# Kernel tuning notes

Hardware: AMD Instinct MI355X
Metric: run time of the kernel (lower is better)

## Reference

```python
import jax, jax.numpy as jnp
import numpy as np

B, T, C, H, D = 2, 2048, 1024, 16, 64

def setup_inputs() -> dict:
    key = jax.random.key(0)
    ks = jax.random.split(key, 5)
    s = 1.0 / np.sqrt(C)
    return {
        "hidden_states": jax.random.normal(ks[0], (B, T, C), jnp.float32),
        "Wq": jax.random.normal(ks[1], (H, C, D), jnp.float32) * s,
        "Wk": jax.random.normal(ks[2], (H, C, D), jnp.float32) * s,
        "Wv": jax.random.normal(ks[3], (H, C, D), jnp.float32) * s,
        "Wo": jax.random.normal(ks[4], (C, C), jnp.float32) * s,
    }

def reference(hidden_states, Wq, Wk, Wv, Wo):
    x = hidden_states  # (B, T, C)
    q = jnp.einsum("btc,hcd->bhtd", x, Wq)
    k = jnp.einsum("btc,hcd->bhtd", x, Wk)
    v = jnp.einsum("btc,hcd->bhtd", x, Wv)
    scale = 1.0 / jnp.sqrt(jnp.asarray(D, x.dtype))
    scores = jnp.einsum("bhtd,bhsd->bhts", q, k) * scale  # (B,H,T,T)
    Tlen = x.shape[1]
    causal = jnp.tril(jnp.ones((Tlen, Tlen), bool))
    scores = jnp.where(causal, scores, jnp.asarray(-jnp.inf, x.dtype))
    probs = jax.nn.softmax(scores, axis=-1)
    heads = jnp.einsum("bhts,bhsd->bhtd", probs, v)  # (B,H,T,D)
    concat = heads.transpose(0, 2, 1, 3).reshape(x.shape[0], Tlen, H * D)  # (B,T,C)
    return jnp.einsum("btc,oc->bto", concat, Wo)  # output projection (dropout=0)
```

## Files before the change

### kernel.cpp

```cpp
#include <hip/hip_runtime.h>
#include <math.h>

#define B_ 2
#define T_ 2048
#define C_ 1024
#define H_ 16
#define D_ 64

typedef short short8 __attribute__((ext_vector_type(8)));
typedef float f32x4 __attribute__((ext_vector_type(4)));
typedef float f32x16 __attribute__((ext_vector_type(16)));

#define LOG2E 1.44269504088896f

__device__ __forceinline__ unsigned short f2bf(float f) {
    unsigned int u = __float_as_uint(f);
    u += 0x7FFFu + ((u >> 16) & 1u);
    return (unsigned short)(u >> 16);
}

#define NCAST 2560

__global__ __launch_bounds__(256) void prep_all(
    const float* __restrict__ x,  const float* __restrict__ Wq,
    const float* __restrict__ Wk, const float* __restrict__ Wv,
    const float* __restrict__ Wo,
    unsigned short* __restrict__ xb,   unsigned short* __restrict__ Wall,
    unsigned short* __restrict__ wob,  int nX, int nW)
{
    const int bid = blockIdx.x;
    const int tid = threadIdx.x;
    if (bid < NCAST) {
        int i = (bid * 256 + tid) * 8;
        const float* s;
        unsigned short* d;
        if (i < nX) { s = x + i; d = xb + i; }
        else {
            int j = i - nX;
            if (j >= nW) return;
            s = Wo + j; d = wob + j;
        }
        float4 a = *(const float4*)s;
        float4 b = *(const float4*)(s + 4);
        ushort4 o0, o1;
        o0.x = f2bf(a.x); o0.y = f2bf(a.y); o0.z = f2bf(a.z); o0.w = f2bf(a.w);
        o1.x = f2bf(b.x); o1.y = f2bf(b.y); o1.z = f2bf(b.z); o1.w = f2bf(b.w);
        *(ushort4*)d = o0;
        *(ushort4*)(d + 4) = o1;
        return;
    }
    __shared__ float t[64][65];
    const int tb = bid - NCAST;
    const int c0 = (tb & 15) * 64;
    const int h  = (tb >> 4) & 15;
    const int z  = tb >> 8;
    const float* W = (z == 0) ? Wq : (z == 1) ? Wk : Wv;
    unsigned short* Wt = Wall + (size_t)z * H_ * D_ * C_;
    const int r = tid >> 4, c4 = (tid & 15) * 4;
    #pragma unroll
    for (int p = 0; p < 4; p++) {
        int cl = r + p * 16;
        float4 v = *(const float4*)&W[((size_t)h * C_ + c0 + cl) * D_ + c4];
        t[cl][c4 + 0] = v.x; t[cl][c4 + 1] = v.y;
        t[cl][c4 + 2] = v.z; t[cl][c4 + 3] = v.w;
    }
    __syncthreads();
    #pragma unroll
    for (int p = 0; p < 4; p++) {
        int d = r + p * 16;
        ushort4 o;
        o.x = f2bf(t[c4 + 0][d]); o.y = f2bf(t[c4 + 1][d]);
        o.z = f2bf(t[c4 + 2][d]); o.w = f2bf(t[c4 + 3][d]);
        *(ushort4*)&Wt[((size_t)h * D_ + d) * C_ + c0 + c4] = o;
    }
}

__global__ __launch_bounds__(256) void qkv_big(
    const unsigned short* __restrict__ X,
    const unsigned short* __restrict__ Wall,
    unsigned short* __restrict__ Qo,
    unsigned short* __restrict__ Ko,
    unsigned short* __restrict__ Vt)
{
    __shared__ unsigned short As[128][72];
    __shared__ unsigned short Bs[128][72];

    const int m0 = blockIdx.x * 128;
    const int n0 = blockIdx.y * 128;
    const int z  = n0 >> 10;
    const int tid = threadIdx.x;
    const int w = tid >> 6, lane = tid & 63, quad = lane >> 4, l16 = lane & 15;
    const int wm = w & 1, wn = w >> 1;
    const int lrow = tid >> 3, lcol = (tid & 7) * 8;

    f32x4 acc[4][4] = {};

    short8 ar[4], br[4];
    #pragma unroll
    for (int p = 0; p < 4; p++) {
        int r = lrow + p * 32;
        ar[p] = *(const short8*)&X[(size_t)(m0 + r) * C_ + lcol];
        br[p] = *(const short8*)&Wall[(size_t)(n0 + r) * C_ + lcol];
    }

    for (int k0 = 0; k0 < C_; k0 += 64) {
        __syncthreads();
        #pragma unroll
        for (int p = 0; p < 4; p++) {
            int r = lrow + p * 32;
            *(short8*)&As[r][lcol] = ar[p];
            *(short8*)&Bs[r][lcol] = br[p];
        }
        __syncthreads();
        if (k0 + 64 < C_) {
            #pragma unroll
            for (int p = 0; p < 4; p++) {
                int r = lrow + p * 32;
                ar[p] = *(const short8*)&X[(size_t)(m0 + r) * C_ + k0 + 64 + lcol];
                br[p] = *(const short8*)&Wall[(size_t)(n0 + r) * C_ + k0 + 64 + lcol];
            }
        }
        #pragma unroll
        for (int ks = 0; ks < 2; ks++) {
            short8 af[4], bf[4];
            #pragma unroll
            for (int i = 0; i < 4; i++)
                af[i] = *(const short8*)&As[wm * 64 + i * 16 + l16][ks * 32 + quad * 8];
            #pragma unroll
            for (int j = 0; j < 4; j++)
                bf[j] = *(const short8*)&Bs[wn * 64 + j * 16 + l16][ks * 32 + quad * 8];
            #pragma unroll
            for (int i = 0; i < 4; i++)
                #pragma unroll
                for (int j = 0; j < 4; j++)
                    acc[i][j] = __builtin_amdgcn_mfma_f32_16x16x32_bf16(af[i], bf[j], acc[i][j], 0, 0, 0);
        }
    }

    if (z == 2) {
        #pragma unroll
        for (int j = 0; j < 4; j++) {
            const int n = n0 + wn * 64 + j * 16 + l16;
            const int h = (n >> 6) & 15, d = n & 63;
            #pragma unroll
            for (int i = 0; i < 4; i++) {
                const int m = m0 + wm * 64 + i * 16 + quad * 4;
                const int b = m >> 11, t = m & (T_ - 1);
                ushort4 pk;
                pk.x = f2bf(acc[i][j][0]);
                pk.y = f2bf(acc[i][j][1]);
                pk.z = f2bf(acc[i][j][2]);
                pk.w = f2bf(acc[i][j][3]);
                *(ushort4*)&Vt[(((size_t)b * H_ + h) * D_ + d) * T_ + t] = pk;
            }
        }
    } else {
        const float scale = (z == 0) ? 0.125f * LOG2E : 1.0f;
        unsigned short* O = (z == 0) ? Qo : Ko;
        #pragma unroll
        for (int j = 0; j < 4; j++) {
            const int n = n0 + wn * 64 + j * 16 + l16;
            const int h = (n >> 6) & 15, d = n & 63;
            #pragma unroll
            for (int i = 0; i < 4; i++)
                #pragma unroll
                for (int r = 0; r < 4; r++) {
                    const int m = m0 + wm * 64 + i * 16 + quad * 4 + r;
                    const int b = m >> 11, t = m & (T_ - 1);
                    O[(((size_t)b * H_ + h) * T_ + t) * D_ + d] = f2bf(acc[i][j][r] * scale);
                }
        }
    }
}

__global__ __launch_bounds__(512, 2) void flash_mfma(
    const unsigned short* __restrict__ Q,
    const unsigned short* __restrict__ K,
    const unsigned short* __restrict__ Vt,
    unsigned short* __restrict__ CC)
{
    __shared__ unsigned short kst[64][72];
    __shared__ unsigned short vts[64][72];
    __shared__ float fob[128][68];
    __shared__ float flb_p[128];
    __shared__ float flb_t[128];

    const int dd   = blockIdx.x;
    const int xs   = dd & 7;
    const int loc  = dd >> 3;
    const int head = xs * 4 + (loc & 3);
    const int p    = loc >> 2;
    const int h = head & 15, b = head >> 4;

    const int tid = threadIdx.x;
    const int w = tid >> 6, lane = tid & 63;
    const int l31 = lane & 31, hi = lane >> 5;
    const int sw = (w & 1) * 32;
    const int qw = (w >> 1) * 32;
    const int lrow = tid >> 3, lcol = (tid & 7) * 8;
    const size_t hb  = ((size_t)b * H_ + h) * T_;
    const size_t hbD = ((size_t)b * H_ + h) * D_;

    for (int ph = 0; ph < 2; ph++) {
        const int qb = ph ? (15 - p) : p;
        const int q0 = qb * 128;
        const int niter = 2 * qb + 2;

        short8 qf[4];
        #pragma unroll
        for (int k4 = 0; k4 < 4; k4++)
            qf[k4] = *(const short8*)&Q[(hb + q0 + qw + l31) * D_ + k4 * 16 + hi * 8];

        float l_lane = 0.0f;
        f32x16 o0 = {}, o1 = {};

        short8 kreg, vreg;
        kreg = *(const short8*)&K[(hb + lrow) * D_ + lcol];
        vreg = *(const short8*)&Vt[(hbD + lrow) * T_ + lcol];

        for (int kb = 0; kb < niter; kb++) {
            __syncthreads();
            *(short8*)&kst[lrow][lcol] = kreg;
            *(short8*)&vts[lrow][lcol] = vreg;
            __syncthreads();
            if (kb + 1 < niter) {
                const int k0n = (kb + 1) * 64;
                kreg = *(const short8*)&K[(hb + k0n + lrow) * D_ + lcol];
                vreg = *(const short8*)&Vt[(hbD + lrow) * T_ + k0n + lcol];
            }

            const int s0 = kb * 64 + sw;
            if (s0 > q0 + qw + 31) continue;

            f32x16 S = {};
            __builtin_amdgcn_s_setprio(1);
            #pragma unroll
            for (int k4 = 0; k4 < 4; k4++) {
                short8 kf = *(const short8*)&kst[sw + l31][k4 * 16 + hi * 8];
                S = __builtin_amdgcn_mfma_f32_32x32x16_bf16(kf, qf[k4], S, 0, 0, 0);
            }
            __builtin_amdgcn_s_setprio(0);

            if (kb >= 2 * qb) {
                const int sg = s0 - q0 - qw;
                #pragma unroll
                for (int reg = 0; reg < 16; reg++) {
                    const int srel = (reg & 3) + 4 * hi + 8 * (reg >> 2);
                    if (sg + srel > l31) S[reg] = -INFINITY;
                }
            }

            unsigned Wd[8];
            #pragma unroll
            for (int blk = 0; blk < 4; blk++) {
                float e0 = exp2f(S[4 * blk + 0]);
                float e1 = exp2f(S[4 * blk + 1]);
                float e2 = exp2f(S[4 * blk + 2]);
                float e3 = exp2f(S[4 * blk + 3]);
                l_lane += (e0 + e1) + (e2 + e3);
                Wd[2 * blk + 0] = __builtin_amdgcn_perm(
                    __float_as_uint(e1) + 0x8000u, __float_as_uint(e0) + 0x8000u, 0x07060302u);
                Wd[2 * blk + 1] = __builtin_amdgcn_perm(
                    __float_as_uint(e3) + 0x8000u, __float_as_uint(e2) + 0x8000u, 0x07060302u);
            }

            unsigned a0 = Wd[0], b0 = Wd[2];
            asm("v_permlane32_swap_b32 %0, %1" : "+v"(a0), "+v"(b0));
            unsigned a1 = Wd[1], b1 = Wd[3];
            asm("v_permlane32_swap_b32 %0, %1" : "+v"(a1), "+v"(b1));
            unsigned c0 = Wd[4], d0 = Wd[6];
            asm("v_permlane32_swap_b32 %0, %1" : "+v"(c0), "+v"(d0));
            unsigned c1 = Wd[5], d1 = Wd[7];
            asm("v_permlane32_swap_b32 %0, %1" : "+v"(c1), "+v"(d1));
            union { unsigned u[4]; short8 v; } pw0, pw1;
            pw0.u[0] = a0; pw0.u[1] = a1; pw0.u[2] = b0; pw0.u[3] = b1;
            pw1.u[0] = c0; pw1.u[1] = c1; pw1.u[2] = d0; pw1.u[3] = d1;

            __builtin_amdgcn_s_setprio(1);
            {
                short8 vf;
                vf = *(const short8*)&vts[l31][sw + hi * 8];
                o0 = __builtin_amdgcn_mfma_f32_32x32x16_bf16(pw0.v, vf, o0, 0, 0, 0);
                vf = *(const short8*)&vts[l31][sw + 16 + hi * 8];
                o0 = __builtin_amdgcn_mfma_f32_32x32x16_bf16(pw1.v, vf, o0, 0, 0, 0);
                vf = *(const short8*)&vts[32 + l31][sw + hi * 8];
                o1 = __builtin_amdgcn_mfma_f32_32x32x16_bf16(pw0.v, vf, o1, 0, 0, 0);
                vf = *(const short8*)&vts[32 + l31][sw + 16 + hi * 8];
                o1 = __builtin_amdgcn_mfma_f32_32x32x16_bf16(pw1.v, vf, o1, 0, 0, 0);
            }
            __builtin_amdgcn_s_setprio(0);
        }

        l_lane += __shfl_xor(l_lane, 32);

        if (w & 1) {
            if (lane < 32) flb_p[qw + lane] = l_lane;
            #pragma unroll
            for (int reg = 0; reg < 16; reg++) {
                const int qr = (reg & 3) + 4 * hi + 8 * (reg >> 2);
                fob[qw + qr][l31]      = o0[reg];
                fob[qw + qr][32 + l31] = o1[reg];
            }
        }
        __syncthreads();
        if (!(w & 1)) {
            const float lt = l_lane + flb_p[qw + l31];
            if (lane < 32) flb_t[qw + lane] = lt;
            #pragma unroll
            for (int reg = 0; reg < 16; reg++) {
                const int qr = (reg & 3) + 4 * hi + 8 * (reg >> 2);
                const float invl = 1.0f / flb_t[qw + qr];
                const float v0 = o0[reg] + fob[qw + qr][l31];
                const float v1 = o1[reg] + fob[qw + qr][32 + l31];
                const int t = q0 + qw + qr;
                CC[((size_t)b * T_ + t) * C_ + h * D_ + l31]      = f2bf(v0 * invl);
                CC[((size_t)b * T_ + t) * C_ + h * D_ + 32 + l31] = f2bf(v1 * invl);
            }
        }
    }
}

__global__ __launch_bounds__(256) void out_big(
    const unsigned short* __restrict__ X,
    const unsigned short* __restrict__ Wob,
    float* __restrict__ out)
{
    __shared__ unsigned short As[128][72];
    __shared__ unsigned short Bs[128][72];

    const int m0 = blockIdx.x * 128;
    const int n0 = blockIdx.y * 128;
    const int tid = threadIdx.x;
    const int w = tid >> 6, lane = tid & 63, quad = lane >> 4, l16 = lane & 15;
    const int wm = w & 1, wn = w >> 1;
    const int lrow = tid >> 3, lcol = (tid & 7) * 8;

    f32x4 acc[4][4] = {};

    short8 ar[4], br[4];
    #pragma unroll
    for (int p = 0; p < 4; p++) {
        int r = lrow + p * 32;
        ar[p] = *(const short8*)&X[(size_t)(m0 + r) * C_ + lcol];
        br[p] = *(const short8*)&Wob[(size_t)(n0 + r) * C_ + lcol];
    }

    for (int k0 = 0; k0 < C_; k0 += 64) {
        __syncthreads();
        #pragma unroll
        for (int p = 0; p < 4; p++) {
            int r = lrow + p * 32;
            *(short8*)&As[r][lcol] = ar[p];
            *(short8*)&Bs[r][lcol] = br[p];
        }
        __syncthreads();
        if (k0 + 64 < C_) {
            #pragma unroll
            for (int p = 0; p < 4; p++) {
                int r = lrow + p * 32;
                ar[p] = *(const short8*)&X[(size_t)(m0 + r) * C_ + k0 + 64 + lcol];
                br[p] = *(const short8*)&Wob[(size_t)(n0 + r) * C_ + k0 + 64 + lcol];
            }
        }
        #pragma unroll
        for (int ks = 0; ks < 2; ks++) {
            short8 af[4], bf[4];
            #pragma unroll
            for (int i = 0; i < 4; i++)
                af[i] = *(const short8*)&As[wm * 64 + i * 16 + l16][ks * 32 + quad * 8];
            #pragma unroll
            for (int j = 0; j < 4; j++)
                bf[j] = *(const short8*)&Bs[wn * 64 + j * 16 + l16][ks * 32 + quad * 8];
            #pragma unroll
            for (int i = 0; i < 4; i++)
                #pragma unroll
                for (int j = 0; j < 4; j++)
                    acc[i][j] = __builtin_amdgcn_mfma_f32_16x16x32_bf16(af[i], bf[j], acc[i][j], 0, 0, 0);
        }
    }

    #pragma unroll
    for (int i = 0; i < 4; i++)
        #pragma unroll
        for (int j = 0; j < 4; j++)
            #pragma unroll
            for (int r = 0; r < 4; r++)
                out[(size_t)(m0 + wm * 64 + i * 16 + quad * 4 + r) * C_ + n0 + wn * 64 + j * 16 + l16] = acc[i][j][r];
}

extern "C" void kernel_launch(void* const* d_in, const int* in_sizes, int n_in,
                              void* d_out, int out_size, void* d_ws, size_t ws_size,
                              hipStream_t stream) {
    const float* x  = (const float*)d_in[0];
    const float* Wq = (const float*)d_in[1];
    const float* Wk = (const float*)d_in[2];
    const float* Wv = (const float*)d_in[3];
    const float* Wo = (const float*)d_in[4];
    float* out = (float*)d_out;

    const size_t nX = (size_t)B_ * T_ * C_;
    const size_t nW = (size_t)H_ * C_ * D_;
    const size_t nQ = (size_t)B_ * H_ * T_ * D_;
    unsigned short* xb   = (unsigned short*)d_ws;
    unsigned short* Wall = xb + nX;
    unsigned short* Wob  = Wall + 3 * nW;
    unsigned short* Qb   = Wob + nW;
    unsigned short* Kb   = Qb + nQ;
    unsigned short* Vtb  = Kb + nQ;
    unsigned short* CCb  = Vtb + nQ;

    prep_all<<<dim3(NCAST + 768), 256, 0, stream>>>(
        x, Wq, Wk, Wv, Wo, xb, Wall, Wob, (int)nX, (int)nW);
    qkv_big<<<dim3(32, 24), 256, 0, stream>>>(xb, Wall, Qb, Kb, Vtb);
    flash_mfma<<<dim3(256), 512, 0, stream>>>(Qb, Kb, Vtb, CCb);
    out_big<<<dim3(32, 8), 256, 0, stream>>>(CCb, Wob, out);
}
```

Baseline: 172.4 us.

## Split flash attention into 64-row query blocks with 256-thread workgroups

The flash attention kernel moves from 256 workgroups of 512 threads, each handling two paired 128-row query blocks, to 1024 workgroups of 256 threads, each handling a single 64-row query block. Causal load balance now comes from the launch order, which alternates query blocks in a zig-zag across the grid, instead of pairing blocks inside one workgroup. Each thread stages two rows of K and V per tile. Per-tile work for each wave stays the same, but there are more, smaller workgroups, giving more occupancy and finer scheduling at the cost of more redundant K/V loads per query row.

```diff
diff --git a/kernel.cpp b/kernel.cpp
--- a/kernel.cpp
+++ b/kernel.cpp
@@ -173,7 +173,7 @@
     }
 }
 
-__global__ __launch_bounds__(512, 2) void flash_mfma(
+__global__ __launch_bounds__(256, 4) void flash_mfma(
     const unsigned short* __restrict__ Q,
     const unsigned short* __restrict__ K,
     const unsigned short* __restrict__ Vt,
@@ -181,15 +181,17 @@
 {
     __shared__ unsigned short kst[64][72];
     __shared__ unsigned short vts[64][72];
-    __shared__ float fob[128][68];
-    __shared__ float flb_p[128];
-    __shared__ float flb_t[128];
-
-    const int dd   = blockIdx.x;
-    const int xs   = dd & 7;
-    const int loc  = dd >> 3;
-    const int head = xs * 4 + (loc & 3);
-    const int p    = loc >> 2;
+    __shared__ float fob[64][68];
+    __shared__ float flb_p[64];
+    __shared__ float flb_t[64];
+
+    const int dd  = blockIdx.x;
+    const int xs  = dd & 7;
+    const int loc = dd >> 3;
+    const int r4  = loc >> 5;
+    const int c   = loc & 31;
+    const int qb  = (r4 & 1) ? (31 - c) : c;
+    const int head = xs * 4 + r4;
     const int h = head & 15, b = head >> 4;
 
     const int tid = threadIdx.x;
@@ -201,121 +203,127 @@
     const size_t hb  = ((size_t)b * H_ + h) * T_;
     const size_t hbD = ((size_t)b * H_ + h) * D_;
 
-    for (int ph = 0; ph < 2; ph++) {
-        const int qb = ph ? (15 - p) : p;
-        const int q0 = qb * 128;
-        const int niter = 2 * qb + 2;
-
-        short8 qf[4];
-        #pragma unroll
-        for (int k4 = 0; k4 < 4; k4++)
-            qf[k4] = *(const short8*)&Q[(hb + q0 + qw + l31) * D_ + k4 * 16 + hi * 8];
-
-        float l_lane = 0.0f;
-        f32x16 o0 = {}, o1 = {};
-
-        short8 kreg, vreg;
-        kreg = *(const short8*)&K[(hb + lrow) * D_ + lcol];
-        vreg = *(const short8*)&Vt[(hbD + lrow) * T_ + lcol];
-
-        for (int kb = 0; kb < niter; kb++) {
-            __syncthreads();
-            *(short8*)&kst[lrow][lcol] = kreg;
-            *(short8*)&vts[lrow][lcol] = vreg;
-            __syncthreads();
-            if (kb + 1 < niter) {
-                const int k0n = (kb + 1) * 64;
-                kreg = *(const short8*)&K[(hb + k0n + lrow) * D_ + lcol];
-                vreg = *(const short8*)&Vt[(hbD + lrow) * T_ + k0n + lcol];
+    const int q0  = qb * 64;
+    const int nkb = qb + 1;
+
+    short8 qf[4];
+    #pragma unroll
+    for (int k4 = 0; k4 < 4; k4++)
+        qf[k4] = *(const short8*)&Q[(hb + q0 + qw + l31) * D_ + k4 * 16 + hi * 8];
+
+    float l_lane = 0.0f;
+    f32x16 o0 = {}, o1 = {};
+
+    short8 kreg[2], vreg[2];
+    #pragma unroll
+    for (int p = 0; p < 2; p++) {
+        const int r = lrow + p * 32;
+        kreg[p] = *(const short8*)&K[(hb + r) * D_ + lcol];
+        vreg[p] = *(const short8*)&Vt[(hbD + r) * T_ + lcol];
+    }
+
+    for (int kb = 0; kb < nkb; kb++) {
+        __syncthreads();
+        #pragma unroll
+        for (int p = 0; p < 2; p++) {
+            const int r = lrow + p * 32;
+            *(short8*)&kst[r][lcol] = kreg[p];
+            *(short8*)&vts[r][lcol] = vreg[p];
+        }
+        __syncthreads();
+        if (kb + 1 < nkb) {
+            const int k0n = (kb + 1) * 64;
+            #pragma unroll
+            for (int p = 0; p < 2; p++) {
+                const int r = lrow + p * 32;
+                kreg[p] = *(const short8*)&K[(hb + k0n + r) * D_ + lcol];
+                vreg[p] = *(const short8*)&Vt[(hbD + r) * T_ + k0n + lcol];
             }
-
-            const int s0 = kb * 64 + sw;
-            if (s0 > q0 + qw + 31) continue;
-
-            f32x16 S = {};
-            __builtin_amdgcn_s_setprio(1);
-            #pragma unroll
-            for (int k4 = 0; k4 < 4; k4++) {
-                short8 kf = *(const short8*)&kst[sw + l31][k4 * 16 + hi * 8];
-                S = __builtin_amdgcn_mfma_f32_32x32x16_bf16(kf, qf[k4], S, 0, 0, 0);
+        }
+
+        f32x16 S = {};
+        __builtin_amdgcn_s_setprio(1);
+        #pragma unroll
+        for (int k4 = 0; k4 < 4; k4++) {
+            short8 kf = *(const short8*)&kst[sw + l31][k4 * 16 + hi * 8];
+            S = __builtin_amdgcn_mfma_f32_32x32x16_bf16(kf, qf[k4], S, 0, 0, 0);
+        }
+        __builtin_amdgcn_s_setprio(0);
+
+        if (kb == qb) {
+            #pragma unroll
+            for (int reg = 0; reg < 16; reg++) {
+                const int srel = (reg & 3) + 4 * hi + 8 * (reg >> 2);
+                if (sw + srel > qw + l31) S[reg] = -INFINITY;
             }
-            __builtin_amdgcn_s_setprio(0);
-
-            if (kb >= 2 * qb) {
-                const int sg = s0 - q0 - qw;
-                #pragma unroll
-                for (int reg = 0; reg < 16; reg++) {
-                    const int srel = (reg & 3) + 4 * hi + 8 * (reg >> 2);
-                    if (sg + srel > l31) S[reg] = -INFINITY;
-                }
-            }
-
-            unsigned Wd[8];
-            #pragma unroll
-            for (int blk = 0; blk < 4; blk++) {
-                float e0 = exp2f(S[4 * blk + 0]);
-                float e1 = exp2f(S[4 * blk + 1]);
-                float e2 = exp2f(S[4 * blk + 2]);
-                float e3 = exp2f(S[4 * blk + 3]);
-                l_lane += (e0 + e1) + (e2 + e3);
-                Wd[2 * blk + 0] = __builtin_amdgcn_perm(
-                    __float_as_uint(e1) + 0x8000u, __float_as_uint(e0) + 0x8000u, 0x07060302u);
-                Wd[2 * blk + 1] = __builtin_amdgcn_perm(
-                    __float_as_uint(e3) + 0x8000u, __float_as_uint(e2) + 0x8000u, 0x07060302u);
-            }
-
-            unsigned a0 = Wd[0], b0 = Wd[2];
-            asm("v_permlane32_swap_b32 %0, %1" : "+v"(a0), "+v"(b0));
-            unsigned a1 = Wd[1], b1 = Wd[3];
-            asm("v_permlane32_swap_b32 %0, %1" : "+v"(a1), "+v"(b1));
-            unsigned c0 = Wd[4], d0 = Wd[6];
-            asm("v_permlane32_swap_b32 %0, %1" : "+v"(c0), "+v"(d0));
-            unsigned c1 = Wd[5], d1 = Wd[7];
-            asm("v_permlane32_swap_b32 %0, %1" : "+v"(c1), "+v"(d1));
-            union { unsigned u[4]; short8 v; } pw0, pw1;
-            pw0.u[0] = a0; pw0.u[1] = a1; pw0.u[2] = b0; pw0.u[3] = b1;
-            pw1.u[0] = c0; pw1.u[1] = c1; pw1.u[2] = d0; pw1.u[3] = d1;
-
-            __builtin_amdgcn_s_setprio(1);
-            {
-                short8 vf;
-                vf = *(const short8*)&vts[l31][sw + hi * 8];
-                o0 = __builtin_amdgcn_mfma_f32_32x32x16_bf16(pw0.v, vf, o0, 0, 0, 0);
-                vf = *(const short8*)&vts[l31][sw + 16 + hi * 8];
-                o0 = __builtin_amdgcn_mfma_f32_32x32x16_bf16(pw1.v, vf, o0, 0, 0, 0);
-                vf = *(const short8*)&vts[32 + l31][sw + hi * 8];
-                o1 = __builtin_amdgcn_mfma_f32_32x32x16_bf16(pw0.v, vf, o1, 0, 0, 0);
-                vf = *(const short8*)&vts[32 + l31][sw + 16 + hi * 8];
-                o1 = __builtin_amdgcn_mfma_f32_32x32x16_bf16(pw1.v, vf, o1, 0, 0, 0);
-            }
-            __builtin_amdgcn_s_setprio(0);
-        }
-
-        l_lane += __shfl_xor(l_lane, 32);
-
-        if (w & 1) {
-            if (lane < 32) flb_p[qw + lane] = l_lane;
-            #pragma unroll
-            for (int reg = 0; reg < 16; reg++) {
-                const int qr = (reg & 3) + 4 * hi + 8 * (reg >> 2);
-                fob[qw + qr][l31]      = o0[reg];
-                fob[qw + qr][32 + l31] = o1[reg];
-            }
-        }
-        __syncthreads();
-        if (!(w & 1)) {
-            const float lt = l_lane + flb_p[qw + l31];
-            if (lane < 32) flb_t[qw + lane] = lt;
-            #pragma unroll
-            for (int reg = 0; reg < 16; reg++) {
-                const int qr = (reg & 3) + 4 * hi + 8 * (reg >> 2);
-                const float invl = 1.0f / flb_t[qw + qr];
-                const float v0 = o0[reg] + fob[qw + qr][l31];
-                const float v1 = o1[reg] + fob[qw + qr][32 + l31];
-                const int t = q0 + qw + qr;
-                CC[((size_t)b * T_ + t) * C_ + h * D_ + l31]      = f2bf(v0 * invl);
-                CC[((size_t)b * T_ + t) * C_ + h * D_ + 32 + l31] = f2bf(v1 * invl);
-            }
+        }
+
+        unsigned Wd[8];
+        #pragma unroll
+        for (int blk = 0; blk < 4; blk++) {
+            float e0 = exp2f(S[4 * blk + 0]);
+            float e1 = exp2f(S[4 * blk + 1]);
+            float e2 = exp2f(S[4 * blk + 2]);
+            float e3 = exp2f(S[4 * blk + 3]);
+            l_lane += (e0 + e1) + (e2 + e3);
+            Wd[2 * blk + 0] = __builtin_amdgcn_perm(
+                __float_as_uint(e1) + 0x8000u, __float_as_uint(e0) + 0x8000u, 0x07060302u);
+            Wd[2 * blk + 1] = __builtin_amdgcn_perm(
+                __float_as_uint(e3) + 0x8000u, __float_as_uint(e2) + 0x8000u, 0x07060302u);
+        }
+
+        unsigned a0 = Wd[0], b0 = Wd[2];
+        asm("v_permlane32_swap_b32 %0, %1" : "+v"(a0), "+v"(b0));
+        unsigned a1 = Wd[1], b1 = Wd[3];
+        asm("v_permlane32_swap_b32 %0, %1" : "+v"(a1), "+v"(b1));
+        unsigned c0 = Wd[4], d0 = Wd[6];
+        asm("v_permlane32_swap_b32 %0, %1" : "+v"(c0), "+v"(d0));
+        unsigned c1 = Wd[5], d1 = Wd[7];
+        asm("v_permlane32_swap_b32 %0, %1" : "+v"(c1), "+v"(d1));
+        union { unsigned u[4]; short8 v; } pw0, pw1;
+        pw0.u[0] = a0; pw0.u[1] = a1; pw0.u[2] = b0; pw0.u[3] = b1;
+        pw1.u[0] = c0; pw1.u[1] = c1; pw1.u[2] = d0; pw1.u[3] = d1;
+
+        __builtin_amdgcn_s_setprio(1);
+        {
+            short8 vf;
+            vf = *(const short8*)&vts[l31][sw + hi * 8];
+            o0 = __builtin_amdgcn_mfma_f32_32x32x16_bf16(pw0.v, vf, o0, 0, 0, 0);
+            vf = *(const short8*)&vts[l31][sw + 16 + hi * 8];
+            o0 = __builtin_amdgcn_mfma_f32_32x32x16_bf16(pw1.v, vf, o0, 0, 0, 0);
+            vf = *(const short8*)&vts[32 + l31][sw + hi * 8];
+            o1 = __builtin_amdgcn_mfma_f32_32x32x16_bf16(pw0.v, vf, o1, 0, 0, 0);
+            vf = *(const short8*)&vts[32 + l31][sw + 16 + hi * 8];
+            o1 = __builtin_amdgcn_mfma_f32_32x32x16_bf16(pw1.v, vf, o1, 0, 0, 0);
+        }
+        __builtin_amdgcn_s_setprio(0);
+    }
+
+    l_lane += __shfl_xor(l_lane, 32);
+
+    __syncthreads();
+    if (w & 1) {
+        if (lane < 32) flb_p[qw + lane] = l_lane;
+        #pragma unroll
+        for (int reg = 0; reg < 16; reg++) {
+            const int qr = (reg & 3) + 4 * hi + 8 * (reg >> 2);
+            fob[qw + qr][l31]      = o0[reg];
+            fob[qw + qr][32 + l31] = o1[reg];
+        }
+    }
+    __syncthreads();
+    if (!(w & 1)) {
+        const float lt = l_lane + flb_p[qw + l31];
+        if (lane < 32) flb_t[qw + lane] = lt;
+        #pragma unroll
+        for (int reg = 0; reg < 16; reg++) {
+            const int qr = (reg & 3) + 4 * hi + 8 * (reg >> 2);
+            const float invl = 1.0f / flb_t[qw + qr];
+            const float v0 = o0[reg] + fob[qw + qr][l31];
+            const float v1 = o1[reg] + fob[qw + qr][32 + l31];
+            const int t = q0 + qw + qr;
+            CC[((size_t)b * T_ + t) * C_ + h * D_ + l31]      = f2bf(v0 * invl);
+            CC[((size_t)b * T_ + t) * C_ + h * D_ + 32 + l31] = f2bf(v1 * invl);
         }
     }
 }
@@ -412,6 +420,6 @@
     prep_all<<<dim3(NCAST + 768), 256, 0, stream>>>(
         x, Wq, Wk, Wv, Wo, xb, Wall, Wob, (int)nX, (int)nW);
     qkv_big<<<dim3(32, 24), 256, 0, stream>>>(xb, Wall, Qb, Kb, Vtb);
-    flash_mfma<<<dim3(256), 512, 0, stream>>>(Qb, Kb, Vtb, CCb);
+    flash_mfma<<<dim3(1024), 256, 0, stream>>>(Qb, Kb, Vtb, CCb);
     out_big<<<dim3(32, 8), 256, 0, stream>>>(CCb, Wob, out);
 }
```

After: 171.0 us. About the same (-0.8%).
